# Optimization experiments

Hardware: AMD Instinct MI355X
Metric: run time of the kernel (lower is better)

Reference implementation:

```python
import jax, jax.numpy as jnp
import numpy as np

N = 100000   # occupied voxels
C = 128      # input_dim
G = 64       # voxel grid extent per axis


def _build_neighbor_map(rng):
    # random unique voxel coords in a G^3 grid + hash lookup for 3x3x3 offsets
    lin = rng.choice(G ** 3, size=N, replace=False)
    coords = np.stack(np.unravel_index(lin, (G, G, G)), axis=1).astype(np.int64)  # [N,3]
    lut = np.full(G ** 3, -1, np.int32)
    lut[lin] = np.arange(N, dtype=np.int32)
    o = np.arange(-1, 2)
    offs = np.stack(np.meshgrid(o, o, o, indexing='ij'), -1).reshape(27, 3)  # [27,3]
    nc = coords[None, :, :] + offs[:, None, :]                 # [27,N,3]
    valid = ((nc >= 0) & (nc < G)).all(-1)                     # [27,N]
    nlin = (nc[..., 0] * G + nc[..., 1]) * G + nc[..., 2]
    nbr = np.where(valid, lut[np.clip(nlin, 0, G ** 3 - 1)], -1).astype(np.int32)
    return nbr


def setup_inputs() -> dict:
    rng = np.random.default_rng(0)
    nbr = _build_neighbor_map(rng)
    key = jax.random.key(0)
    ks = jax.random.split(key, 5)
    h = C // 2
    x = jax.random.normal(ks[0], (N, C), jnp.float32)
    w1 = jax.random.normal(ks[1], (C, C), jnp.float32) * 0.05
    b1 = jnp.zeros((C,), jnp.float32)
    w2 = jax.random.normal(ks[2], (C, C), jnp.float32) * 0.05
    b2 = jnp.zeros((C,), jnp.float32)
    rw1 = jax.random.normal(ks[3], (27, h, h), jnp.float32) * 0.05
    rb1 = jnp.zeros((h,), jnp.float32)
    rw2 = jax.random.normal(ks[4], (27, h, h), jnp.float32) * 0.05
    rb2 = jnp.zeros((h,), jnp.float32)
    return dict(x=x, w1=w1, b1=b1, w2=w2, b2=b2,
                rw1=rw1, rb1=rb1, rw2=rw2, rb2=rb2,
                nbr=jnp.asarray(nbr))


def _sconv3(feat, nbr, W, b):
    # sparse 3x3x3 conv: gather neighbor features per kernel offset, GEMM, sum
    mask = (nbr >= 0).astype(feat.dtype)                  # [27,N]
    g = feat[jnp.maximum(nbr, 0)] * mask[:, :, None]      # [27,N,c]
    return jnp.einsum('knc,kcd->nd', g, W) + b            # [N,c]


def reference(x, w1, b1, w2, b2, rw1, rb1, rw2, rb2, nbr):
    h = x.shape[1] // 2
    y = x @ w1 + b1                                       # conv1 (1x1x1)
    conv_x, trans_x = y[:, :h], y[:, h:]                  # split
    # resblock (stride 1 -> no skip conv): relu(conv)->relu(conv) + identity
    r = jax.nn.relu(_sconv3(conv_x, nbr, rw1, rb1))
    r = jax.nn.relu(_sconv3(r, nbr, rw2, rb2))
    conv_x = (r + conv_x) + conv_x                        # resblock(x) + x
    # CodedVTRBlock source unavailable: modeled as identity on trans branch
    res = jnp.concatenate([conv_x, trans_x], axis=1) @ w2 + b2  # conv2 (1x1x1)
    return x + res
```

## Files before the change

kernel.cpp:

```cpp
#include <hip/hip_runtime.h>


#define N_PTS 100000
#define NBLK128 782

typedef __attribute__((ext_vector_type(8))) short frag_ab;
typedef __attribute__((ext_vector_type(4))) float f32x4;
#define ZFRAG frag_ab{0, 0, 0, 0, 0, 0, 0, 0}

__device__ __forceinline__ unsigned short f2bf(float f) {
  union { float f; unsigned int i; } v; v.f = f;
  unsigned int r = v.i + 0x7fffu + ((v.i >> 16) & 1u);
  return (unsigned short)(r >> 16);
}
__device__ __forceinline__ float bf2f(unsigned short u) {
  union { unsigned int i; float f; } v; v.i = ((unsigned int)u) << 16; return v.f;
}

__device__ __forceinline__ void gload_lds16(const unsigned short* g, unsigned short* l) {
  __builtin_amdgcn_global_load_lds(
      (const __attribute__((address_space(1))) unsigned int*)g,
      (__attribute__((address_space(3))) unsigned int*)(unsigned int)(size_t)l,
      16, 0, 0);
}

__global__ __launch_bounds__(256) void k_prep(
    const float* __restrict__ w1, const float* __restrict__ w2,
    const float* __restrict__ rw1, const float* __restrict__ rw2,
    unsigned short* __restrict__ w1T, unsigned short* __restrict__ w2T,
    unsigned short* __restrict__ rw1T, unsigned short* __restrict__ rw2T) {
  int t = blockIdx.x * 256 + threadIdx.x;
  if (t < 128 * 128) {
    int c = t >> 7, d = t & 127;
    int pos = d * 128 + ((((c >> 3) ^ (d & 15)) << 3) | (c & 7));
    w1T[pos] = f2bf(w1[t]);
    w2T[pos] = f2bf(w2[t]);
  }
  if (t < 27 * 64 * 64) {
    int k = t >> 12, r = t & 4095, c = r >> 6, d = r & 63;
    int pos = (k << 12) + d * 64 + ((((c >> 3) ^ (d & 7)) << 3) | (c & 7));
    rw1T[pos] = f2bf(rw1[t]);
    rw2T[pos] = f2bf(rw2[t]);
  }
}

__global__ __launch_bounds__(256) void k_gemm_in(
    const float* __restrict__ x, const unsigned short* __restrict__ w1T,
    const float* __restrict__ b1, unsigned short* __restrict__ y) {
  __shared__ unsigned short sw[16384];
  const int tid = threadIdx.x, lane = tid & 63, w = tid >> 6;
  const int m16 = lane & 15, q = lane >> 4;
#pragma unroll
  for (int r = 0; r < 8; ++r) {
    const int off = (w * 8 + r) * 512 + lane * 8;
    gload_lds16(w1T + off, &sw[off]);
  }
  __syncthreads();
  const int rowbase = blockIdx.x * 128 + w * 32;
  f32x4 acc[2][8] = {};
#pragma unroll
  for (int kk = 0; kk < 4; ++kk) {
    frag_ab a[2];
#pragma unroll
    for (int rt = 0; rt < 2; ++rt) {
      int r0 = rowbase + rt * 16 + m16;
      int rc = r0 < N_PTS ? r0 : N_PTS - 1;
      const float* xp = x + (size_t)rc * 128 + kk * 32 + q * 8;
      float4 f0 = *(const float4*)xp;
      float4 f1 = *(const float4*)(xp + 4);
      frag_ab t;
      t[0] = (short)f2bf(f0.x); t[1] = (short)f2bf(f0.y);
      t[2] = (short)f2bf(f0.z); t[3] = (short)f2bf(f0.w);
      t[4] = (short)f2bf(f1.x); t[5] = (short)f2bf(f1.y);
      t[6] = (short)f2bf(f1.z); t[7] = (short)f2bf(f1.w);
      a[rt] = t;
    }
#pragma unroll
    for (int ct = 0; ct < 8; ++ct) {
      const int d = ct * 16 + m16;
      const int phys = ((kk << 2) | q) ^ m16;
      frag_ab bf = *(const frag_ab*)(&sw[d * 128 + phys * 8]);
      acc[0][ct] = __builtin_amdgcn_mfma_f32_16x16x32_bf16(a[0], bf, acc[0][ct], 0, 0, 0);
      acc[1][ct] = __builtin_amdgcn_mfma_f32_16x16x32_bf16(a[1], bf, acc[1][ct], 0, 0, 0);
    }
  }
#pragma unroll
  for (int ct = 0; ct < 8; ++ct) {
    const int col = ct * 16 + m16;
    const float bias = b1[col];
#pragma unroll
    for (int rt = 0; rt < 2; ++rt)
#pragma unroll
      for (int j = 0; j < 4; ++j) {
        int r = rowbase + rt * 16 + q * 4 + j;
        if (r < N_PTS) y[(size_t)r * 128 + col] = f2bf(acc[rt][ct][j] + bias);
      }
  }
}

template <bool FUSE>
__global__ __launch_bounds__(256) void k_conv(
    const unsigned short* __restrict__ feat, const int fstride,
    const int* __restrict__ nbr,
    const unsigned short* __restrict__ rwT, const float* __restrict__ rb,
    const unsigned short* __restrict__ res, unsigned short* __restrict__ out) {
  __shared__ unsigned short sw[2][4096];
  const int tid = threadIdx.x, lane = tid & 63, w = tid >> 6;
  const int m16 = lane & 15, q = lane >> 4;
  const int rowbase = blockIdx.x * 128 + w * 32;
  const int p0 = rowbase + m16, p1 = p0 + 16;
  const bool v0 = p0 < N_PTS, v1 = p1 < N_PTS;
  const int s0 = w * 1024 + lane * 8;
  const int s1 = s0 + 512;

  int i0r[2], i1r[2];
  i0r[0] = v0 ? nbr[p0] : -1;
  i1r[0] = v1 ? nbr[p1] : -1;
  i0r[1] = v0 ? nbr[N_PTS + p0] : -1;
  i1r[1] = v1 ? nbr[N_PTS + p1] : -1;

  frag_ab A[2][2][2];
#pragma unroll
  for (int a = 0; a < 2; ++a)
#pragma unroll
    for (int b = 0; b < 2; ++b)
#pragma unroll
      for (int c = 0; c < 2; ++c) A[a][b][c] = ZFRAG;

  {
    const unsigned short* src = rwT;
    gload_lds16(src + s0, &sw[0][s0]);
    gload_lds16(src + s1, &sw[0][s1]);
    if (i0r[0] >= 0) {
      const unsigned short* fp = feat + (size_t)i0r[0] * fstride + q * 8;
      A[0][0][0] = *(const frag_ab*)fp; A[0][0][1] = *(const frag_ab*)(fp + 32);
    }
    if (i1r[0] >= 0) {
      const unsigned short* fp = feat + (size_t)i1r[0] * fstride + q * 8;
      A[0][1][0] = *(const frag_ab*)fp; A[0][1][1] = *(const frag_ab*)(fp + 32);
    }
  }
  __syncthreads();

  f32x4 acc[2][4] = {};
#pragma unroll
  for (int k = 0; k < 27; ++k) {
    const int b = k & 1;
    if (k + 1 < 27) {
      const unsigned short* src = rwT + ((k + 1) << 12);
      gload_lds16(src + s0, &sw[b ^ 1][s0]);
      gload_lds16(src + s1, &sw[b ^ 1][s1]);
      const int n = (k + 1) & 1;
      int j0 = i0r[n], j1 = i1r[n];
      A[n][0][0] = ZFRAG; A[n][0][1] = ZFRAG; A[n][1][0] = ZFRAG; A[n][1][1] = ZFRAG;
      if (j0 >= 0) {
        const unsigned short* fp = feat + (size_t)j0 * fstride + q * 8;
        A[n][0][0] = *(const frag_ab*)fp; A[n][0][1] = *(const frag_ab*)(fp + 32);
      }
      if (j1 >= 0) {
        const unsigned short* fp = feat + (size_t)j1 * fstride + q * 8;
        A[n][1][0] = *(const frag_ab*)fp; A[n][1][1] = *(const frag_ab*)(fp + 32);
      }
    }
    if (k + 2 < 27) {
      i0r[k & 1] = v0 ? nbr[(k + 2) * N_PTS + p0] : -1;
      i1r[k & 1] = v1 ? nbr[(k + 2) * N_PTS + p1] : -1;
    }
#pragma unroll
    for (int kk = 0; kk < 2; ++kk)
#pragma unroll
      for (int ct = 0; ct < 4; ++ct) {
        const int d = ct * 16 + m16;
        const int phys = ((kk << 2) | q) ^ (m16 & 7);
        frag_ab bf = *(const frag_ab*)(&sw[b][d * 64 + phys * 8]);
        acc[0][ct] = __builtin_amdgcn_mfma_f32_16x16x32_bf16(A[b][0][kk], bf, acc[0][ct], 0, 0, 0);
        acc[1][ct] = __builtin_amdgcn_mfma_f32_16x16x32_bf16(A[b][1][kk], bf, acc[1][ct], 0, 0, 0);
      }
    __syncthreads();
  }

#pragma unroll
  for (int ct = 0; ct < 4; ++ct) {
    const int col = ct * 16 + m16;
    const float bias = rb[col];
#pragma unroll
    for (int rt = 0; rt < 2; ++rt)
#pragma unroll
      for (int j = 0; j < 4; ++j) {
        const int r = rowbase + rt * 16 + q * 4 + j;
        if (r < N_PTS) {
          float v = acc[rt][ct][j] + bias;
          v = v > 0.f ? v : 0.f;
          if constexpr (FUSE) v += 2.f * bf2f(res[(size_t)r * 128 + col]);
          out[(size_t)r * 64 + col] = f2bf(v);
        }
      }
  }
}

__global__ __launch_bounds__(256) void k_gemm_out(
    const float* __restrict__ x, const unsigned short* __restrict__ z1,
    const unsigned short* __restrict__ y, const unsigned short* __restrict__ w2T,
    const float* __restrict__ b2, float* __restrict__ out) {
  __shared__ unsigned short sw[16384];
  const int tid = threadIdx.x, lane = tid & 63, w = tid >> 6;
  const int m16 = lane & 15, q = lane >> 4;
#pragma unroll
  for (int r = 0; r < 8; ++r) {
    const int off = (w * 8 + r) * 512 + lane * 8;
    gload_lds16(w2T + off, &sw[off]);
  }
  __syncthreads();
  const int rowbase = blockIdx.x * 128 + w * 32;
  f32x4 acc[2][8] = {};
#pragma unroll
  for (int kk = 0; kk < 4; ++kk) {
    frag_ab a[2];
#pragma unroll
    for (int rt = 0; rt < 2; ++rt) {
      int r0 = rowbase + rt * 16 + m16;
      int rc = r0 < N_PTS ? r0 : N_PTS - 1;
      const unsigned short* ap = (kk < 2)
          ? (z1 + (size_t)rc * 64 + kk * 32 + q * 8)
          : (y + (size_t)rc * 128 + 64 + (kk - 2) * 32 + q * 8);
      a[rt] = *(const frag_ab*)ap;
    }
#pragma unroll
    for (int ct = 0; ct < 8; ++ct) {
      const int d = ct * 16 + m16;
      const int phys = ((kk << 2) | q) ^ m16;
      frag_ab bf = *(const frag_ab*)(&sw[d * 128 + phys * 8]);
      acc[0][ct] = __builtin_amdgcn_mfma_f32_16x16x32_bf16(a[0], bf, acc[0][ct], 0, 0, 0);
      acc[1][ct] = __builtin_amdgcn_mfma_f32_16x16x32_bf16(a[1], bf, acc[1][ct], 0, 0, 0);
    }
  }
#pragma unroll
  for (int ct = 0; ct < 8; ++ct) {
    const int col = ct * 16 + m16;
    const float bias = b2[col];
#pragma unroll
    for (int rt = 0; rt < 2; ++rt)
#pragma unroll
      for (int j = 0; j < 4; ++j) {
        int r = rowbase + rt * 16 + q * 4 + j;
        if (r < N_PTS) {
          size_t o = (size_t)r * 128 + col;
          out[o] = acc[rt][ct][j] + bias + x[o];
        }
      }
  }
}

extern "C" void kernel_launch(void* const* d_in, const int* in_sizes, int n_in,
                              void* d_out, int out_size, void* d_ws, size_t ws_size,
                              hipStream_t stream) {
  const float* x   = (const float*)d_in[0];
  const float* w1  = (const float*)d_in[1];
  const float* b1  = (const float*)d_in[2];
  const float* w2  = (const float*)d_in[3];
  const float* b2  = (const float*)d_in[4];
  const float* rw1 = (const float*)d_in[5];
  const float* rb1 = (const float*)d_in[6];
  const float* rw2 = (const float*)d_in[7];
  const float* rb2 = (const float*)d_in[8];
  const int* nbr = (const int*)d_in[9];
  float* out = (float*)d_out;

  char* ws = (char*)d_ws;
  unsigned short* w1T  = (unsigned short*)(ws);
  unsigned short* w2T  = (unsigned short*)(ws + 32768);
  unsigned short* rw1T = (unsigned short*)(ws + 65536);
  unsigned short* rw2T = (unsigned short*)(ws + 286720);
  unsigned short* y    = (unsigned short*)(ws + 507904);
  unsigned short* r1   = (unsigned short*)(ws + 507904 + 25600000);
  unsigned short* z1   = (unsigned short*)(ws + 507904 + 38400000);

  k_prep<<<432, 256, 0, stream>>>(w1, w2, rw1, rw2, w1T, w2T, rw1T, rw2T);
  k_gemm_in<<<NBLK128, 256, 0, stream>>>(x, w1T, b1, y);
  k_conv<false><<<NBLK128, 256, 0, stream>>>(y, 128, nbr, rw1T, rb1, nullptr, r1);
  k_conv<true><<<NBLK128, 256, 0, stream>>>(r1, 64, nbr, rw2T, rb2, y, z1);
  k_gemm_out<<<NBLK128, 256, 0, stream>>>(x, z1, y, w2T, b2, out);
}
```

Before: 242.4 us.

## Restructure sparse conv to 2 waves x 64 rows, two kernel offsets per stage

```diff
diff --git a/kernel.cpp b/kernel.cpp
--- a/kernel.cpp
+++ b/kernel.cpp
@@ -55,19 +55,26 @@
     const int off = (w * 8 + r) * 512 + lane * 8;
     gload_lds16(w1T + off, &sw[off]);
   }
-  __syncthreads();
   const int rowbase = blockIdx.x * 128 + w * 32;
-  f32x4 acc[2][8] = {};
-#pragma unroll
-  for (int kk = 0; kk < 4; ++kk) {
-    frag_ab a[2];
+  float4 xr[4][2][2];
+#pragma unroll
+  for (int kk = 0; kk < 4; ++kk)
 #pragma unroll
     for (int rt = 0; rt < 2; ++rt) {
       int r0 = rowbase + rt * 16 + m16;
       int rc = r0 < N_PTS ? r0 : N_PTS - 1;
       const float* xp = x + (size_t)rc * 128 + kk * 32 + q * 8;
-      float4 f0 = *(const float4*)xp;
-      float4 f1 = *(const float4*)(xp + 4);
+      xr[kk][rt][0] = *(const float4*)xp;
+      xr[kk][rt][1] = *(const float4*)(xp + 4);
+    }
+  __syncthreads();
+  f32x4 acc[2][8] = {};
+#pragma unroll
+  for (int kk = 0; kk < 4; ++kk) {
+    frag_ab a[2];
+#pragma unroll
+    for (int rt = 0; rt < 2; ++rt) {
+      float4 f0 = xr[kk][rt][0], f1 = xr[kk][rt][1];
       frag_ab t;
       t[0] = (short)f2bf(f0.x); t[1] = (short)f2bf(f0.y);
       t[2] = (short)f2bf(f0.z); t[3] = (short)f2bf(f0.w);
@@ -99,103 +106,121 @@
 }
 
 template <bool FUSE>
-__global__ __launch_bounds__(256) void k_conv(
+__global__ __launch_bounds__(128) void k_conv(
     const unsigned short* __restrict__ feat, const int fstride,
     const int* __restrict__ nbr,
     const unsigned short* __restrict__ rwT, const float* __restrict__ rb,
     const unsigned short* __restrict__ res, unsigned short* __restrict__ out) {
-  __shared__ unsigned short sw[2][4096];
+  __shared__ unsigned short sw[2][8192];
   const int tid = threadIdx.x, lane = tid & 63, w = tid >> 6;
   const int m16 = lane & 15, q = lane >> 4;
-  const int rowbase = blockIdx.x * 128 + w * 32;
-  const int p0 = rowbase + m16, p1 = p0 + 16;
-  const bool v0 = p0 < N_PTS, v1 = p1 < N_PTS;
-  const int s0 = w * 1024 + lane * 8;
-  const int s1 = s0 + 512;
-
-  int i0r[2], i1r[2];
-  i0r[0] = v0 ? nbr[p0] : -1;
-  i1r[0] = v1 ? nbr[p1] : -1;
-  i0r[1] = v0 ? nbr[N_PTS + p0] : -1;
-  i1r[1] = v1 ? nbr[N_PTS + p1] : -1;
-
-  frag_ab A[2][2][2];
-#pragma unroll
-  for (int a = 0; a < 2; ++a)
-#pragma unroll
-    for (int b = 0; b < 2; ++b)
-#pragma unroll
-      for (int c = 0; c < 2; ++c) A[a][b][c] = ZFRAG;
-
+  const int rowbase = blockIdx.x * 128 + w * 64;
+  int p[4]; bool v[4];
+#pragma unroll
+  for (int s = 0; s < 4; ++s) { p[s] = rowbase + s * 16 + m16; v[s] = p[s] < N_PTS; }
+
+  int idxr[4][4];
+#pragma unroll
+  for (int k = 0; k < 4; ++k)
+#pragma unroll
+    for (int s = 0; s < 4; ++s)
+      idxr[k][s] = v[s] ? nbr[k * N_PTS + p[s]] : -1;
+
+  frag_ab A[2][2][4][2];
+#pragma unroll
+  for (int ks = 0; ks < 2; ++ks)
+#pragma unroll
+    for (int s = 0; s < 4; ++s) {
+      A[0][ks][s][0] = ZFRAG; A[0][ks][s][1] = ZFRAG;
+      int ix = idxr[ks][s];
+      if (ix >= 0) {
+        const unsigned short* fp = feat + (size_t)ix * fstride + q * 8;
+        A[0][ks][s][0] = *(const frag_ab*)fp;
+        A[0][ks][s][1] = *(const frag_ab*)(fp + 32);
+      }
+    }
   {
-    const unsigned short* src = rwT;
-    gload_lds16(src + s0, &sw[0][s0]);
-    gload_lds16(src + s1, &sw[0][s1]);
-    if (i0r[0] >= 0) {
-      const unsigned short* fp = feat + (size_t)i0r[0] * fstride + q * 8;
-      A[0][0][0] = *(const frag_ab*)fp; A[0][0][1] = *(const frag_ab*)(fp + 32);
-    }
-    if (i1r[0] >= 0) {
-      const unsigned short* fp = feat + (size_t)i1r[0] * fstride + q * 8;
-      A[0][1][0] = *(const frag_ab*)fp; A[0][1][1] = *(const frag_ab*)(fp + 32);
+#pragma unroll
+    for (int r = 0; r < 8; ++r) {
+      const int off = (r * 128 + tid) * 8;
+      gload_lds16(rwT + off, &sw[0][off]);
     }
   }
   __syncthreads();
 
-  f32x4 acc[2][4] = {};
-#pragma unroll
-  for (int k = 0; k < 27; ++k) {
-    const int b = k & 1;
-    if (k + 1 < 27) {
-      const unsigned short* src = rwT + ((k + 1) << 12);
-      gload_lds16(src + s0, &sw[b ^ 1][s0]);
-      gload_lds16(src + s1, &sw[b ^ 1][s1]);
-      const int n = (k + 1) & 1;
-      int j0 = i0r[n], j1 = i1r[n];
-      A[n][0][0] = ZFRAG; A[n][0][1] = ZFRAG; A[n][1][0] = ZFRAG; A[n][1][1] = ZFRAG;
-      if (j0 >= 0) {
-        const unsigned short* fp = feat + (size_t)j0 * fstride + q * 8;
-        A[n][0][0] = *(const frag_ab*)fp; A[n][0][1] = *(const frag_ab*)(fp + 32);
-      }
-      if (j1 >= 0) {
-        const unsigned short* fp = feat + (size_t)j1 * fstride + q * 8;
-        A[n][1][0] = *(const frag_ab*)fp; A[n][1][1] = *(const frag_ab*)(fp + 32);
-      }
-    }
-    if (k + 2 < 27) {
-      i0r[k & 1] = v0 ? nbr[(k + 2) * N_PTS + p0] : -1;
-      i1r[k & 1] = v1 ? nbr[(k + 2) * N_PTS + p1] : -1;
-    }
-#pragma unroll
-    for (int kk = 0; kk < 2; ++kk)
-#pragma unroll
-      for (int ct = 0; ct < 4; ++ct) {
-        const int d = ct * 16 + m16;
-        const int phys = ((kk << 2) | q) ^ (m16 & 7);
-        frag_ab bf = *(const frag_ab*)(&sw[b][d * 64 + phys * 8]);
-        acc[0][ct] = __builtin_amdgcn_mfma_f32_16x16x32_bf16(A[b][0][kk], bf, acc[0][ct], 0, 0, 0);
-        acc[1][ct] = __builtin_amdgcn_mfma_f32_16x16x32_bf16(A[b][1][kk], bf, acc[1][ct], 0, 0, 0);
-      }
+  f32x4 acc[4][4] = {};
+  for (int g = 0; g < 14; ++g) {
+    const int gb = g & 1;
+    if (g < 13) {
+      const unsigned short* src = rwT + ((2 * g + 2) << 12);
+#pragma unroll
+      for (int r = 0; r < 8; ++r) {
+        const int off = (r * 128 + tid) * 8;
+        gload_lds16(src + off, &sw[gb ^ 1][off]);
+      }
+#pragma unroll
+      for (int ks = 0; ks < 2; ++ks) {
+        const int kn = 2 * g + 2 + ks;
+#pragma unroll
+        for (int s = 0; s < 4; ++s) {
+          A[gb ^ 1][ks][s][0] = ZFRAG; A[gb ^ 1][ks][s][1] = ZFRAG;
+          if (kn < 27) {
+            int ix = idxr[kn & 3][s];
+            if (ix >= 0) {
+              const unsigned short* fp = feat + (size_t)ix * fstride + q * 8;
+              A[gb ^ 1][ks][s][0] = *(const frag_ab*)fp;
+              A[gb ^ 1][ks][s][1] = *(const frag_ab*)(fp + 32);
+            }
+          }
+        }
+      }
+#pragma unroll
+      for (int d = 0; d < 2; ++d) {
+        const int kf = 2 * g + 4 + d;
+        if (kf < 27)
+#pragma unroll
+          for (int s = 0; s < 4; ++s)
+            idxr[kf & 3][s] = v[s] ? nbr[kf * N_PTS + p[s]] : -1;
+      }
+    }
+#pragma unroll
+    for (int ks = 0; ks < 2; ++ks) {
+      const int k = 2 * g + ks;
+      if (k < 27) {
+#pragma unroll
+        for (int kk = 0; kk < 2; ++kk)
+#pragma unroll
+          for (int ct = 0; ct < 4; ++ct) {
+            const int d = ct * 16 + m16;
+            const int phys = ((kk << 2) | q) ^ (m16 & 7);
+            frag_ab bf = *(const frag_ab*)(&sw[gb][ks * 4096 + d * 64 + phys * 8]);
+#pragma unroll
+            for (int s = 0; s < 4; ++s)
+              acc[s][ct] = __builtin_amdgcn_mfma_f32_16x16x32_bf16(
+                  A[gb][ks][s][kk], bf, acc[s][ct], 0, 0, 0);
+          }
+      }
+    }
     __syncthreads();
   }
 
 #pragma unroll
-  for (int ct = 0; ct < 4; ++ct) {
-    const int col = ct * 16 + m16;
-    const float bias = rb[col];
-#pragma unroll
-    for (int rt = 0; rt < 2; ++rt)
+  for (int s = 0; s < 4; ++s)
+#pragma unroll
+    for (int ct = 0; ct < 4; ++ct) {
+      const int col = ct * 16 + m16;
+      const float bias = rb[col];
 #pragma unroll
       for (int j = 0; j < 4; ++j) {
-        const int r = rowbase + rt * 16 + q * 4 + j;
+        const int r = rowbase + s * 16 + q * 4 + j;
         if (r < N_PTS) {
-          float v = acc[rt][ct][j] + bias;
-          v = v > 0.f ? v : 0.f;
-          if constexpr (FUSE) v += 2.f * bf2f(res[(size_t)r * 128 + col]);
-          out[(size_t)r * 64 + col] = f2bf(v);
+          float val = acc[s][ct][j] + bias;
+          val = val > 0.f ? val : 0.f;
+          if constexpr (FUSE) val += 2.f * bf2f(res[(size_t)r * 128 + col]);
+          out[(size_t)r * 64 + col] = f2bf(val);
         }
       }
-  }
+    }
 }
 
 __global__ __launch_bounds__(256) void k_gemm_out(
@@ -210,12 +235,10 @@
     const int off = (w * 8 + r) * 512 + lane * 8;
     gload_lds16(w2T + off, &sw[off]);
   }
-  __syncthreads();
   const int rowbase = blockIdx.x * 128 + w * 32;
-  f32x4 acc[2][8] = {};
-#pragma unroll
-  for (int kk = 0; kk < 4; ++kk) {
-    frag_ab a[2];
+  frag_ab a[4][2];
+#pragma unroll
+  for (int kk = 0; kk < 4; ++kk)
 #pragma unroll
     for (int rt = 0; rt < 2; ++rt) {
       int r0 = rowbase + rt * 16 + m16;
@@ -223,17 +246,20 @@
       const unsigned short* ap = (kk < 2)
           ? (z1 + (size_t)rc * 64 + kk * 32 + q * 8)
           : (y + (size_t)rc * 128 + 64 + (kk - 2) * 32 + q * 8);
-      a[rt] = *(const frag_ab*)ap;
-    }
+      a[kk][rt] = *(const frag_ab*)ap;
+    }
+  __syncthreads();
+  f32x4 acc[2][8] = {};
+#pragma unroll
+  for (int kk = 0; kk < 4; ++kk)
 #pragma unroll
     for (int ct = 0; ct < 8; ++ct) {
       const int d = ct * 16 + m16;
       const int phys = ((kk << 2) | q) ^ m16;
       frag_ab bf = *(const frag_ab*)(&sw[d * 128 + phys * 8]);
-      acc[0][ct] = __builtin_amdgcn_mfma_f32_16x16x32_bf16(a[0], bf, acc[0][ct], 0, 0, 0);
-      acc[1][ct] = __builtin_amdgcn_mfma_f32_16x16x32_bf16(a[1], bf, acc[1][ct], 0, 0, 0);
-    }
-  }
+      acc[0][ct] = __builtin_amdgcn_mfma_f32_16x16x32_bf16(a[kk][0], bf, acc[0][ct], 0, 0, 0);
+      acc[1][ct] = __builtin_amdgcn_mfma_f32_16x16x32_bf16(a[kk][1], bf, acc[1][ct], 0, 0, 0);
+    }
 #pragma unroll
   for (int ct = 0; ct < 8; ++ct) {
     const int col = ct * 16 + m16;
@@ -277,7 +303,7 @@
 
   k_prep<<<432, 256, 0, stream>>>(w1, w2, rw1, rw2, w1T, w2T, rw1T, rw2T);
   k_gemm_in<<<NBLK128, 256, 0, stream>>>(x, w1T, b1, y);
-  k_conv<false><<<NBLK128, 256, 0, stream>>>(y, 128, nbr, rw1T, rb1, nullptr, r1);
-  k_conv<true><<<NBLK128, 256, 0, stream>>>(r1, 64, nbr, rw2T, rb2, y, z1);
+  k_conv<false><<<NBLK128, 128, 0, stream>>>(y, 128, nbr, rw1T, rb1, nullptr, r1);
+  k_conv<true><<<NBLK128, 128, 0, stream>>>(r1, 64, nbr, rw2T, rb2, y, z1);
   k_gemm_out<<<NBLK128, 256, 0, stream>>>(x, z1, y, w2T, b2, out);
 }
```

New measurement: 573.2 us. 2.36x slower.

## Fuse second sparse conv with output GEMM and transpose weights via LDS

Applied to the files above, without the earlier changes.

```diff
diff --git a/kernel.cpp b/kernel.cpp
--- a/kernel.cpp
+++ b/kernel.cpp
@@ -29,18 +29,51 @@
     const float* __restrict__ rw1, const float* __restrict__ rw2,
     unsigned short* __restrict__ w1T, unsigned short* __restrict__ w2T,
     unsigned short* __restrict__ rw1T, unsigned short* __restrict__ rw2T) {
-  int t = blockIdx.x * 256 + threadIdx.x;
-  if (t < 128 * 128) {
-    int c = t >> 7, d = t & 127;
-    int pos = d * 128 + ((((c >> 3) ^ (d & 15)) << 3) | (c & 7));
-    w1T[pos] = f2bf(w1[t]);
-    w2T[pos] = f2bf(w2[t]);
-  }
-  if (t < 27 * 64 * 64) {
-    int k = t >> 12, r = t & 4095, c = r >> 6, d = r & 63;
-    int pos = (k << 12) + d * 64 + ((((c >> 3) ^ (d & 7)) << 3) | (c & 7));
-    rw1T[pos] = f2bf(rw1[t]);
-    rw2T[pos] = f2bf(rw2[t]);
+  __shared__ unsigned short L[8320];
+  const int tid = threadIdx.x, bid = blockIdx.x;
+  if (bid < 16) {
+    const bool isw1 = (bid < 8);
+    const float* src = isw1 ? w1 : w2;
+    unsigned short* dst = isw1 ? w1T : w2T;
+    const int seg = bid & 7;
+#pragma unroll
+    for (int i = 0; i < 8; ++i) {
+      int idx = i * 256 + tid;
+      int c = idx >> 4, dl = idx & 15;
+      L[c * 17 + dl] = f2bf(src[c * 128 + seg * 16 + dl]);
+    }
+    __syncthreads();
+    const int dl = tid >> 4, j = tid & 15;
+    const int d = seg * 16 + dl;
+    frag_ab v;
+#pragma unroll
+    for (int i = 0; i < 8; ++i) v[i] = (short)L[(8 * j + i) * 17 + dl];
+    const int chunk = isw1 ? (j ^ (d & 15)) : j;
+    *(frag_ab*)(dst + d * 128 + (chunk << 3)) = v;
+  } else {
+    const int k = bid - 16;
+#pragma unroll
+    for (int i = 0; i < 16; ++i) {
+      int idx = i * 256 + tid;
+      int c = idx >> 6, d = idx & 63;
+      L[c * 65 + d] = f2bf(rw1[k * 4096 + idx]);
+      L[4160 + c * 65 + d] = f2bf(rw2[k * 4096 + idx]);
+    }
+    __syncthreads();
+#pragma unroll
+    for (int h = 0; h < 2; ++h) {
+      int cid = h * 256 + tid;
+      int d = cid >> 3, j = cid & 7;
+      frag_ab v1, v2;
+#pragma unroll
+      for (int i = 0; i < 8; ++i) {
+        v1[i] = (short)L[(8 * j + i) * 65 + d];
+        v2[i] = (short)L[4160 + (8 * j + i) * 65 + d];
+      }
+      int pos = k * 4096 + d * 64 + ((j ^ (d & 7)) << 3);
+      *(frag_ab*)(rw1T + pos) = v1;
+      *(frag_ab*)(rw2T + pos) = v2;
+    }
   }
 }
 
@@ -98,12 +131,11 @@
   }
 }
 
-template <bool FUSE>
-__global__ __launch_bounds__(256) void k_conv(
-    const unsigned short* __restrict__ feat, const int fstride,
+__global__ __launch_bounds__(256) void k_conv1(
+    const unsigned short* __restrict__ feat,
     const int* __restrict__ nbr,
     const unsigned short* __restrict__ rwT, const float* __restrict__ rb,
-    const unsigned short* __restrict__ res, unsigned short* __restrict__ out) {
+    unsigned short* __restrict__ out) {
   __shared__ unsigned short sw[2][4096];
   const int tid = threadIdx.x, lane = tid & 63, w = tid >> 6;
   const int m16 = lane & 15, q = lane >> 4;
@@ -112,6 +144,7 @@
   const bool v0 = p0 < N_PTS, v1 = p1 < N_PTS;
   const int s0 = w * 1024 + lane * 8;
   const int s1 = s0 + 512;
+  const int fstride = 128;
 
   int i0r[2], i1r[2];
   i0r[0] = v0 ? nbr[p0] : -1;
@@ -128,9 +161,8 @@
       for (int c = 0; c < 2; ++c) A[a][b][c] = ZFRAG;
 
   {
-    const unsigned short* src = rwT;
-    gload_lds16(src + s0, &sw[0][s0]);
-    gload_lds16(src + s1, &sw[0][s1]);
+    gload_lds16(rwT + s0, &sw[0][s0]);
+    gload_lds16(rwT + s1, &sw[0][s1]);
     if (i0r[0] >= 0) {
       const unsigned short* fp = feat + (size_t)i0r[0] * fstride + q * 8;
       A[0][0][0] = *(const frag_ab*)fp; A[0][0][1] = *(const frag_ab*)(fp + 32);
@@ -191,47 +223,140 @@
         if (r < N_PTS) {
           float v = acc[rt][ct][j] + bias;
           v = v > 0.f ? v : 0.f;
-          if constexpr (FUSE) v += 2.f * bf2f(res[(size_t)r * 128 + col]);
           out[(size_t)r * 64 + col] = f2bf(v);
         }
       }
   }
 }
 
-__global__ __launch_bounds__(256) void k_gemm_out(
-    const float* __restrict__ x, const unsigned short* __restrict__ z1,
-    const unsigned short* __restrict__ y, const unsigned short* __restrict__ w2T,
+__global__ __launch_bounds__(256) void k_conv2_fused(
+    const unsigned short* __restrict__ feat,
+    const int* __restrict__ nbr,
+    const unsigned short* __restrict__ rwT, const float* __restrict__ rb,
+    const unsigned short* __restrict__ y,
+    const float* __restrict__ x, const unsigned short* __restrict__ w2T,
     const float* __restrict__ b2, float* __restrict__ out) {
-  __shared__ unsigned short sw[16384];
+  __shared__ unsigned short sw[2][4096];
+  __shared__ unsigned short zt[128 * 72];
   const int tid = threadIdx.x, lane = tid & 63, w = tid >> 6;
   const int m16 = lane & 15, q = lane >> 4;
-#pragma unroll
-  for (int r = 0; r < 8; ++r) {
-    const int off = (w * 8 + r) * 512 + lane * 8;
-    gload_lds16(w2T + off, &sw[off]);
+  const int rowbase = blockIdx.x * 128 + w * 32;
+  const int p0 = rowbase + m16, p1 = p0 + 16;
+  const bool v0 = p0 < N_PTS, v1 = p1 < N_PTS;
+  const int s0 = w * 1024 + lane * 8;
+  const int s1 = s0 + 512;
+  const int fstride = 64;
+
+  int i0r[2], i1r[2];
+  i0r[0] = v0 ? nbr[p0] : -1;
+  i1r[0] = v1 ? nbr[p1] : -1;
+  i0r[1] = v0 ? nbr[N_PTS + p0] : -1;
+  i1r[1] = v1 ? nbr[N_PTS + p1] : -1;
+
+  frag_ab A[2][2][2];
+#pragma unroll
+  for (int a = 0; a < 2; ++a)
+#pragma unroll
+    for (int b = 0; b < 2; ++b)
+#pragma unroll
+      for (int c = 0; c < 2; ++c) A[a][b][c] = ZFRAG;
+
+  {
+    gload_lds16(rwT + s0, &sw[0][s0]);
+    gload_lds16(rwT + s1, &sw[0][s1]);
+    if (i0r[0] >= 0) {
+      const unsigned short* fp = feat + (size_t)i0r[0] * fstride + q * 8;
+      A[0][0][0] = *(const frag_ab*)fp; A[0][0][1] = *(const frag_ab*)(fp + 32);
+    }
+    if (i1r[0] >= 0) {
+      const unsigned short* fp = feat + (size_t)i1r[0] * fstride + q * 8;
+      A[0][1][0] = *(const frag_ab*)fp; A[0][1][1] = *(const frag_ab*)(fp + 32);
+    }
   }
   __syncthreads();
-  const int rowbase = blockIdx.x * 128 + w * 32;
-  f32x4 acc[2][8] = {};
+
+  f32x4 acc[2][4] = {};
+#pragma unroll
+  for (int k = 0; k < 27; ++k) {
+    const int b = k & 1;
+    if (k + 1 < 27) {
+      const unsigned short* src = rwT + ((k + 1) << 12);
+      gload_lds16(src + s0, &sw[b ^ 1][s0]);
+      gload_lds16(src + s1, &sw[b ^ 1][s1]);
+      const int n = (k + 1) & 1;
+      int j0 = i0r[n], j1 = i1r[n];
+      A[n][0][0] = ZFRAG; A[n][0][1] = ZFRAG; A[n][1][0] = ZFRAG; A[n][1][1] = ZFRAG;
+      if (j0 >= 0) {
+        const unsigned short* fp = feat + (size_t)j0 * fstride + q * 8;
+        A[n][0][0] = *(const frag_ab*)fp; A[n][0][1] = *(const frag_ab*)(fp + 32);
+      }
+      if (j1 >= 0) {
+        const unsigned short* fp = feat + (size_t)j1 * fstride + q * 8;
+        A[n][1][0] = *(const frag_ab*)fp; A[n][1][1] = *(const frag_ab*)(fp + 32);
+      }
+    }
+    if (k + 2 < 27) {
+      i0r[k & 1] = v0 ? nbr[(k + 2) * N_PTS + p0] : -1;
+      i1r[k & 1] = v1 ? nbr[(k + 2) * N_PTS + p1] : -1;
+    }
+#pragma unroll
+    for (int kk = 0; kk < 2; ++kk)
+#pragma unroll
+      for (int ct = 0; ct < 4; ++ct) {
+        const int d = ct * 16 + m16;
+        const int phys = ((kk << 2) | q) ^ (m16 & 7);
+        frag_ab bf = *(const frag_ab*)(&sw[b][d * 64 + phys * 8]);
+        acc[0][ct] = __builtin_amdgcn_mfma_f32_16x16x32_bf16(A[b][0][kk], bf, acc[0][ct], 0, 0, 0);
+        acc[1][ct] = __builtin_amdgcn_mfma_f32_16x16x32_bf16(A[b][1][kk], bf, acc[1][ct], 0, 0, 0);
+      }
+    __syncthreads();
+  }
+
+#pragma unroll
+  for (int ct = 0; ct < 4; ++ct) {
+    const int col = ct * 16 + m16;
+    const float bias = rb[col];
+#pragma unroll
+    for (int rt = 0; rt < 2; ++rt)
+#pragma unroll
+      for (int j = 0; j < 4; ++j) {
+        const int lr = w * 32 + rt * 16 + q * 4 + j;
+        const int r = rowbase + rt * 16 + q * 4 + j;
+        float v = acc[rt][ct][j] + bias;
+        v = v > 0.f ? v : 0.f;
+        float rv = (r < N_PTS) ? bf2f(y[(size_t)r * 128 + col]) : 0.f;
+        zt[lr * 72 + col] = f2bf(v + 2.f * rv);
+      }
+  }
+
+  frag_ab az[2][2];
+#pragma unroll
+  for (int kk = 0; kk < 2; ++kk)
+#pragma unroll
+    for (int rt = 0; rt < 2; ++rt) {
+      const int lr = w * 32 + rt * 16 + m16;
+      az[kk][rt] = *(const frag_ab*)(&zt[lr * 72 + kk * 32 + q * 8]);
+    }
+  frag_ab ay[2][2];
+#pragma unroll
+  for (int kk = 0; kk < 2; ++kk)
+#pragma unroll
+    for (int rt = 0; rt < 2; ++rt) {
+      const int r0 = rowbase + rt * 16 + m16;
+      const int rc = r0 < N_PTS ? r0 : N_PTS - 1;
+      ay[kk][rt] = *(const frag_ab*)(y + (size_t)rc * 128 + 64 + kk * 32 + q * 8);
+    }
+  f32x4 acc2[2][8] = {};
 #pragma unroll
   for (int kk = 0; kk < 4; ++kk) {
-    frag_ab a[2];
-#pragma unroll
-    for (int rt = 0; rt < 2; ++rt) {
-      int r0 = rowbase + rt * 16 + m16;
-      int rc = r0 < N_PTS ? r0 : N_PTS - 1;
-      const unsigned short* ap = (kk < 2)
-          ? (z1 + (size_t)rc * 64 + kk * 32 + q * 8)
-          : (y + (size_t)rc * 128 + 64 + (kk - 2) * 32 + q * 8);
-      a[rt] = *(const frag_ab*)ap;
-    }
+    frag_ab a0 = (kk < 2) ? az[kk][0] : ay[kk - 2][0];
+    frag_ab a1 = (kk < 2) ? az[kk][1] : ay[kk - 2][1];
 #pragma unroll
     for (int ct = 0; ct < 8; ++ct) {
       const int d = ct * 16 + m16;
-      const int phys = ((kk << 2) | q) ^ m16;
-      frag_ab bf = *(const frag_ab*)(&sw[d * 128 + phys * 8]);
-      acc[0][ct] = __builtin_amdgcn_mfma_f32_16x16x32_bf16(a[0], bf, acc[0][ct], 0, 0, 0);
-      acc[1][ct] = __builtin_amdgcn_mfma_f32_16x16x32_bf16(a[1], bf, acc[1][ct], 0, 0, 0);
+      frag_ab bf = *(const frag_ab*)(w2T + (size_t)d * 128 + kk * 32 + q * 8);
+      acc2[0][ct] = __builtin_amdgcn_mfma_f32_16x16x32_bf16(a0, bf, acc2[0][ct], 0, 0, 0);
+      acc2[1][ct] = __builtin_amdgcn_mfma_f32_16x16x32_bf16(a1, bf, acc2[1][ct], 0, 0, 0);
     }
   }
 #pragma unroll
@@ -242,10 +367,10 @@
     for (int rt = 0; rt < 2; ++rt)
 #pragma unroll
       for (int j = 0; j < 4; ++j) {
-        int r = rowbase + rt * 16 + q * 4 + j;
+        const int r = rowbase + rt * 16 + q * 4 + j;
         if (r < N_PTS) {
           size_t o = (size_t)r * 128 + col;
-          out[o] = acc[rt][ct][j] + bias + x[o];
+          out[o] = acc2[rt][ct][j] + bias + x[o];
         }
       }
   }
@@ -273,11 +398,9 @@
   unsigned short* rw2T = (unsigned short*)(ws + 286720);
   unsigned short* y    = (unsigned short*)(ws + 507904);
   unsigned short* r1   = (unsigned short*)(ws + 507904 + 25600000);
-  unsigned short* z1   = (unsigned short*)(ws + 507904 + 38400000);
-
-  k_prep<<<432, 256, 0, stream>>>(w1, w2, rw1, rw2, w1T, w2T, rw1T, rw2T);
+
+  k_prep<<<43, 256, 0, stream>>>(w1, w2, rw1, rw2, w1T, w2T, rw1T, rw2T);
   k_gemm_in<<<NBLK128, 256, 0, stream>>>(x, w1T, b1, y);
-  k_conv<false><<<NBLK128, 256, 0, stream>>>(y, 128, nbr, rw1T, rb1, nullptr, r1);
-  k_conv<true><<<NBLK128, 256, 0, stream>>>(r1, 64, nbr, rw2T, rb2, y, z1);
-  k_gemm_out<<<NBLK128, 256, 0, stream>>>(x, z1, y, w2T, b2, out);
-}
+  k_conv1<<<NBLK128, 256, 0, stream>>>(y, nbr, rw1T, rb1, r1);
+  k_conv2_fused<<<NBLK128, 256, 0, stream>>>(r1, nbr, rw2T, rb2, y, x, w2T, b2, out);
+}
```

Result: slower. 272.4 us (+12.4%).
